# Kernel tuning notes

Measured on AMD Instinct MI355X. Metric: run time of the kernel, lower is better.

Reference implementation:

```python
import jax, jax.numpy as jnp
import numpy as np

SIGMA = 1.0

def setup_inputs() -> dict:
    key = jax.random.key(0)
    k1, k2 = jax.random.split(key)
    N, IN, OUT = 524288, 64, 128
    x = jax.random.normal(k1, (N, IN), dtype=jnp.float32)
    bin_centers = jax.random.normal(k2, (OUT, IN), dtype=jnp.float32)
    return {"x": x, "bin_centers": bin_centers}

def reference(x, bin_centers):
    # distances[n,o] = sum_i (x[n,i] - c[o,i])^2 = ||x_n||^2 - 2 x_n.c_o + ||c_o||^2
    x2 = jnp.sum(x * x, axis=1)[:, None]                # [N,1]
    c2 = jnp.sum(bin_centers * bin_centers, axis=1)[None, :]  # [1,O]
    xc = jnp.einsum('ni,oi->no', x, bin_centers)        # [N,O] GEMM
    distances = x2 - 2.0 * xc + c2                      # [N,O]
    rbf = jnp.exp(-distances / (2.0 * SIGMA ** 2))      # [N,O]
    # histogram[o,i] = sum_n rbf[n,o] * x[n,i]  ->  rbf^T @ x
    histogram = jnp.einsum('no,ni->oi', rbf, x)         # [O,I] GEMM
    return histogram
```

## Files before the change

kernel.cpp:

```cpp
#include <hip/hip_runtime.h>
#include <stdint.h>


typedef __bf16 bf16x8 __attribute__((ext_vector_type(8)));
typedef unsigned short ushortx8 __attribute__((ext_vector_type(8)));
typedef unsigned short ushortx4 __attribute__((ext_vector_type(4)));
typedef float floatx4 __attribute__((ext_vector_type(4)));

#define LOG2E 1.4426950408889634f

#if __has_builtin(__builtin_amdgcn_exp2f)
#define EXP2F(x) __builtin_amdgcn_exp2f(x)
#else
#define EXP2F(x) exp2f(x)
#endif

static __device__ __forceinline__ unsigned short f2bf(float f) {
  unsigned int u = __float_as_uint(f);
  u += 0x7fffu + ((u >> 16) & 1u);
  return (unsigned short)(u >> 16);
}
static __device__ __forceinline__ float bf2f(unsigned short h) {
  return __uint_as_float(((unsigned int)h) << 16);
}

static __device__ __forceinline__ floatx4 mfma_bf16(ushortx8 a, ushortx8 b, floatx4 c) {
  return __builtin_amdgcn_mfma_f32_16x16x32_bf16(
      __builtin_bit_cast(bf16x8, a), __builtin_bit_cast(bf16x8, b), c, 0, 0, 0);
}

#define LSTR 72

__global__ __launch_bounds__(256, 2) void rbf_hist_kernel(
    const float* __restrict__ x, const float* __restrict__ c,
    float* __restrict__ out) {
  __shared__ unsigned short sXhi[64][LSTR];
  __shared__ unsigned short sXlo[64][LSTR];
  __shared__ unsigned short sXT [64][LSTR];
  __shared__ unsigned short sP  [128][LSTR];
  __shared__ float          sX2 [64];

  const int t    = threadIdx.x;
  const int lane = t & 63;
  const int w    = t >> 6;
  const int l15  = lane & 15;
  const int quad = lane >> 4;

  ushortx8 chi[8][2], clo[8][2];
  float c2r[8];
#pragma unroll
  for (int ot = 0; ot < 8; ++ot) {
    float sq = 0.f;
#pragma unroll
    for (int s = 0; s < 2; ++s) {
      const float* p = c + (ot * 16 + l15) * 64 + s * 32 + quad * 8;
      float4 va = *(const float4*)(p);
      float4 vb = *(const float4*)(p + 4);
      float f[8] = {va.x, va.y, va.z, va.w, vb.x, vb.y, vb.z, vb.w};
      ushortx8 hv, lv;
#pragma unroll
      for (int j = 0; j < 8; ++j) {
        sq += f[j] * f[j];
        unsigned short hh = f2bf(f[j]);
        hv[j] = hh;
        lv[j] = f2bf(f[j] - bf2f(hh));
      }
      chi[ot][s] = hv;
      clo[ot][s] = lv;
    }
    sq += __shfl_xor(sq, 16);
    sq += __shfl_xor(sq, 32);
    c2r[ot] = sq;
  }

  floatx4 hacc[2][4];
#pragma unroll
  for (int a = 0; a < 2; ++a)
#pragma unroll
    for (int b = 0; b < 4; ++b) {
      floatx4 z = {0.f, 0.f, 0.f, 0.f};
      hacc[a][b] = z;
    }

  const int row_block = blockIdx.x * 1024;

  const int r = t >> 2, q = t & 3;
  float4 v[4];
#pragma unroll
  for (int g = 0; g < 4; ++g)
    v[g] = *(const float4*)(x + (size_t)(row_block + r) * 64 + q * 4 + g * 16);

  for (int it = 0; it < 16; ++it) {
    __syncthreads();

    {
      float sq = 0.f;
#pragma unroll
      for (int g = 0; g < 4; ++g) {
        const int col = q * 4 + g * 16;
        float f[4] = {v[g].x, v[g].y, v[g].z, v[g].w};
        ushortx4 hv, lv;
#pragma unroll
        for (int j = 0; j < 4; ++j) {
          sq += f[j] * f[j];
          unsigned short hh = f2bf(f[j]);
          hv[j] = hh;
          lv[j] = f2bf(f[j] - bf2f(hh));
          sXT[col + j][r] = hh;
        }
        *(ushortx4*)&sXhi[r][col] = hv;
        *(ushortx4*)&sXlo[r][col] = lv;
      }
      sq += __shfl_xor(sq, 1);
      sq += __shfl_xor(sq, 2);
      if (q == 0) sX2[r] = sq;
    }
    __syncthreads();

    if (it < 15) {
      const size_t nrow = (size_t)(row_block + (it + 1) * 64 + r) * 64;
#pragma unroll
      for (int g = 0; g < 4; ++g)
        v[g] = *(const float4*)(x + nrow + q * 4 + g * 16);
    }

    {
      const int nt = w;
      ushortx8 xh[2], xl[2];
#pragma unroll
      for (int s = 0; s < 2; ++s) {
        xh[s] = *(const ushortx8*)&sXhi[nt * 16 + l15][s * 32 + quad * 8];
        xl[s] = *(const ushortx8*)&sXlo[nt * 16 + l15][s * 32 + quad * 8];
      }
      float x2v[4];
#pragma unroll
      for (int e = 0; e < 4; ++e) x2v[e] = sX2[nt * 16 + quad * 4 + e];

#pragma unroll
      for (int ot = 0; ot < 8; ++ot) {
        floatx4 acc;
#pragma unroll
        for (int e = 0; e < 4; ++e) acc[e] = -0.5f * (x2v[e] + c2r[ot]);
        acc = mfma_bf16(xh[0], chi[ot][0], acc);
        acc = mfma_bf16(xh[1], chi[ot][1], acc);
        acc = mfma_bf16(xh[0], clo[ot][0], acc);
        acc = mfma_bf16(xh[1], clo[ot][1], acc);
        acc = mfma_bf16(xl[0], chi[ot][0], acc);
        acc = mfma_bf16(xl[1], chi[ot][1], acc);
        unsigned short rb[4];
#pragma unroll
        for (int e = 0; e < 4; ++e) rb[e] = f2bf(EXP2F(acc[e] * LOG2E));
        const int o = ot * 16 + l15;
        const int n0 = nt * 16 + quad * 4;
        *(unsigned int*)&sP[o][n0]     = (unsigned int)rb[0] | ((unsigned int)rb[1] << 16);
        *(unsigned int*)&sP[o][n0 + 2] = (unsigned int)rb[2] | ((unsigned int)rb[3] << 16);
      }
    }
    __syncthreads();

#pragma unroll
    for (int s = 0; s < 2; ++s) {
      ushortx8 a0 = *(const ushortx8*)&sP[(2 * w)     * 16 + l15][s * 32 + quad * 8];
      ushortx8 a1 = *(const ushortx8*)&sP[(2 * w + 1) * 16 + l15][s * 32 + quad * 8];
#pragma unroll
      for (int itl = 0; itl < 4; ++itl) {
        ushortx8 b = *(const ushortx8*)&sXT[itl * 16 + l15][s * 32 + quad * 8];
        hacc[0][itl] = mfma_bf16(a0, b, hacc[0][itl]);
        hacc[1][itl] = mfma_bf16(a1, b, hacc[1][itl]);
      }
    }
  }

#pragma unroll
  for (int oi = 0; oi < 2; ++oi)
#pragma unroll
    for (int itl = 0; itl < 4; ++itl)
#pragma unroll
      for (int e = 0; e < 4; ++e) {
        int o = (2 * w + oi) * 16 + quad * 4 + e;
        int i = itl * 16 + l15;
        atomicAdd(out + o * 64 + i, hacc[oi][itl][e]);
      }
}

__global__ void zero_out_kernel(float* out, int n) {
  int i = blockIdx.x * 256 + threadIdx.x;
  if (i < n) out[i] = 0.f;
}

extern "C" void kernel_launch(void* const* d_in, const int* in_sizes, int n_in,
                              void* d_out, int out_size, void* d_ws, size_t ws_size,
                              hipStream_t stream) {
  (void)in_sizes; (void)n_in; (void)d_ws; (void)ws_size;
  const float* x = (const float*)d_in[0];
  const float* c = (const float*)d_in[1];
  float* out = (float*)d_out;

  zero_out_kernel<<<(out_size + 255) / 256, 256, 0, stream>>>(out, out_size);
  rbf_hist_kernel<<<512, 256, 0, stream>>>(x, c, out);
}
```

Baseline: 220.8 us.

## Persistent grid with per-wave O-split and workspace partial reduction

The grid goes from 512 to 768 blocks, which loop over 64-row tiles in grid-stride order, and occupancy rises to 3 blocks per CU. Each wave now holds centers for only its own two output tiles and loops over all four row tiles, so register pressure drops. It also writes its P rows in the same slices it later consumes. When the workspace is large enough, per-block partial histograms go to the workspace and a separate reduce kernel sums them, replacing contended atomics on the output. The costs are an extra kernel launch and about 25 MB of workspace writes and reads.

After: 213.6 us. -3.2%, faster.

```diff
diff --git a/kernel.cpp b/kernel.cpp
--- a/kernel.cpp
+++ b/kernel.cpp
@@ -8,6 +8,8 @@
 typedef float floatx4 __attribute__((ext_vector_type(4)));
 
 #define LOG2E 1.4426950408889634f
+#define GRIDN 768
+#define NTILES 8192
 
 #if __has_builtin(__builtin_amdgcn_exp2f)
 #define EXP2F(x) __builtin_amdgcn_exp2f(x)
@@ -31,9 +33,9 @@
 
 #define LSTR 72
 
-__global__ __launch_bounds__(256, 2) void rbf_hist_kernel(
+__global__ __launch_bounds__(256, 3) void rbf_hist_kernel(
     const float* __restrict__ x, const float* __restrict__ c,
-    float* __restrict__ out) {
+    float* __restrict__ out, float* __restrict__ ws, int use_ws) {
   __shared__ unsigned short sXhi[64][LSTR];
   __shared__ unsigned short sXlo[64][LSTR];
   __shared__ unsigned short sXT [64][LSTR];
@@ -46,10 +48,11 @@
   const int l15  = lane & 15;
   const int quad = lane >> 4;
 
-  ushortx8 chi[8][2], clo[8][2];
-  float c2r[8];
-#pragma unroll
-  for (int ot = 0; ot < 8; ++ot) {
+  ushortx8 chi[2][2], clo[2][2];
+  float c2r[2];
+#pragma unroll
+  for (int oo = 0; oo < 2; ++oo) {
+    const int ot = 2 * w + oo;
     float sq = 0.f;
 #pragma unroll
     for (int s = 0; s < 2; ++s) {
@@ -65,12 +68,12 @@
         hv[j] = hh;
         lv[j] = f2bf(f[j] - bf2f(hh));
       }
-      chi[ot][s] = hv;
-      clo[ot][s] = lv;
+      chi[oo][s] = hv;
+      clo[oo][s] = lv;
     }
     sq += __shfl_xor(sq, 16);
     sq += __shfl_xor(sq, 32);
-    c2r[ot] = sq;
+    c2r[oo] = sq;
   }
 
   floatx4 hacc[2][4];
@@ -82,15 +85,16 @@
       hacc[a][b] = z;
     }
 
-  const int row_block = blockIdx.x * 1024;
-
   const int r = t >> 2, q = t & 3;
   float4 v[4];
-#pragma unroll
-  for (int g = 0; g < 4; ++g)
-    v[g] = *(const float4*)(x + (size_t)(row_block + r) * 64 + q * 4 + g * 16);
-
-  for (int it = 0; it < 16; ++it) {
+  {
+    const size_t row0 = (size_t)(blockIdx.x * 64 + r) * 64;
+#pragma unroll
+    for (int g = 0; g < 4; ++g)
+      v[g] = *(const float4*)(x + row0 + q * 4 + g * 16);
+  }
+
+  for (int tile = blockIdx.x; tile < NTILES; tile += GRIDN) {
     __syncthreads();
 
     {
@@ -115,42 +119,40 @@
       sq += __shfl_xor(sq, 2);
       if (q == 0) sX2[r] = sq;
     }
-    __syncthreads();
-
-    if (it < 15) {
-      const size_t nrow = (size_t)(row_block + (it + 1) * 64 + r) * 64;
+
+    if (tile + GRIDN < NTILES) {
+      const size_t nrow = (size_t)((tile + GRIDN) * 64 + r) * 64;
 #pragma unroll
       for (int g = 0; g < 4; ++g)
         v[g] = *(const float4*)(x + nrow + q * 4 + g * 16);
     }
-
-    {
-      const int nt = w;
-      ushortx8 xh[2], xl[2];
-#pragma unroll
-      for (int s = 0; s < 2; ++s) {
-        xh[s] = *(const ushortx8*)&sXhi[nt * 16 + l15][s * 32 + quad * 8];
-        xl[s] = *(const ushortx8*)&sXlo[nt * 16 + l15][s * 32 + quad * 8];
-      }
+    __syncthreads();
+
+#pragma unroll
+    for (int nt = 0; nt < 4; ++nt) {
+      ushortx8 xh0 = *(const ushortx8*)&sXhi[nt * 16 + l15][quad * 8];
+      ushortx8 xh1 = *(const ushortx8*)&sXhi[nt * 16 + l15][32 + quad * 8];
+      ushortx8 xl0 = *(const ushortx8*)&sXlo[nt * 16 + l15][quad * 8];
+      ushortx8 xl1 = *(const ushortx8*)&sXlo[nt * 16 + l15][32 + quad * 8];
       float x2v[4];
 #pragma unroll
       for (int e = 0; e < 4; ++e) x2v[e] = sX2[nt * 16 + quad * 4 + e];
 
 #pragma unroll
-      for (int ot = 0; ot < 8; ++ot) {
+      for (int oo = 0; oo < 2; ++oo) {
         floatx4 acc;
 #pragma unroll
-        for (int e = 0; e < 4; ++e) acc[e] = -0.5f * (x2v[e] + c2r[ot]);
-        acc = mfma_bf16(xh[0], chi[ot][0], acc);
-        acc = mfma_bf16(xh[1], chi[ot][1], acc);
-        acc = mfma_bf16(xh[0], clo[ot][0], acc);
-        acc = mfma_bf16(xh[1], clo[ot][1], acc);
-        acc = mfma_bf16(xl[0], chi[ot][0], acc);
-        acc = mfma_bf16(xl[1], chi[ot][1], acc);
+        for (int e = 0; e < 4; ++e) acc[e] = -0.5f * (x2v[e] + c2r[oo]);
+        acc = mfma_bf16(xh0, chi[oo][0], acc);
+        acc = mfma_bf16(xh1, chi[oo][1], acc);
+        acc = mfma_bf16(xh0, clo[oo][0], acc);
+        acc = mfma_bf16(xh1, clo[oo][1], acc);
+        acc = mfma_bf16(xl0, chi[oo][0], acc);
+        acc = mfma_bf16(xl1, chi[oo][1], acc);
         unsigned short rb[4];
 #pragma unroll
         for (int e = 0; e < 4; ++e) rb[e] = f2bf(EXP2F(acc[e] * LOG2E));
-        const int o = ot * 16 + l15;
+        const int o = (2 * w + oo) * 16 + l15;
         const int n0 = nt * 16 + quad * 4;
         *(unsigned int*)&sP[o][n0]     = (unsigned int)rb[0] | ((unsigned int)rb[1] << 16);
         *(unsigned int*)&sP[o][n0 + 2] = (unsigned int)rb[2] | ((unsigned int)rb[3] << 16);
@@ -171,16 +173,41 @@
     }
   }
 
-#pragma unroll
-  for (int oi = 0; oi < 2; ++oi)
-#pragma unroll
-    for (int itl = 0; itl < 4; ++itl)
-#pragma unroll
-      for (int e = 0; e < 4; ++e) {
-        int o = (2 * w + oi) * 16 + quad * 4 + e;
-        int i = itl * 16 + l15;
-        atomicAdd(out + o * 64 + i, hacc[oi][itl][e]);
-      }
+  if (use_ws) {
+    float* part = ws + (size_t)blockIdx.x * 8192;
+#pragma unroll
+    for (int oi = 0; oi < 2; ++oi)
+#pragma unroll
+      for (int itl = 0; itl < 4; ++itl)
+#pragma unroll
+        for (int e = 0; e < 4; ++e) {
+          int o = (2 * w + oi) * 16 + quad * 4 + e;
+          int i = itl * 16 + l15;
+          part[o * 64 + i] = hacc[oi][itl][e];
+        }
+  } else {
+#pragma unroll
+    for (int oi = 0; oi < 2; ++oi)
+#pragma unroll
+      for (int itl = 0; itl < 4; ++itl)
+#pragma unroll
+        for (int e = 0; e < 4; ++e) {
+          int o = (2 * w + oi) * 16 + quad * 4 + e;
+          int i = itl * 16 + l15;
+          atomicAdd(out + o * 64 + i, hacc[oi][itl][e]);
+        }
+  }
+}
+
+__global__ void reduce_kernel(const float* __restrict__ ws, float* __restrict__ out) {
+  const int tid = blockIdx.x * 256 + threadIdx.x;
+  const int e = tid & 8191;
+  const int half = tid >> 13;
+  const float* p = ws + (size_t)half * 384 * 8192 + e;
+  float s = 0.f;
+#pragma unroll 8
+  for (int b = 0; b < 384; ++b) s += p[(size_t)b * 8192];
+  atomicAdd(out + e, s);
 }
 
 __global__ void zero_out_kernel(float* out, int n) {
@@ -191,11 +218,16 @@
 extern "C" void kernel_launch(void* const* d_in, const int* in_sizes, int n_in,
                               void* d_out, int out_size, void* d_ws, size_t ws_size,
                               hipStream_t stream) {
-  (void)in_sizes; (void)n_in; (void)d_ws; (void)ws_size;
+  (void)in_sizes; (void)n_in;
   const float* x = (const float*)d_in[0];
   const float* c = (const float*)d_in[1];
   float* out = (float*)d_out;
+  float* ws  = (float*)d_ws;
+
+  const int use_ws = (ws_size >= (size_t)GRIDN * 8192 * sizeof(float)) ? 1 : 0;
 
   zero_out_kernel<<<(out_size + 255) / 256, 256, 0, stream>>>(out, out_size);
-  rbf_hist_kernel<<<512, 256, 0, stream>>>(x, c, out);
-}
+  rbf_hist_kernel<<<GRIDN, 256, 0, stream>>>(x, c, out, ws, use_ws);
+  if (use_ws)
+    reduce_kernel<<<64, 256, 0, stream>>>(ws, out);
+}
```
